# Performance work log

Hardware: AMD Instinct MI355X
Metric: run time of the kernel (lower is better)

The kernel has to match this reference:

```python
import jax, jax.numpy as jnp
import numpy as np

H = 8
LOG2 = 0.6931471805599453  # softplus beta = ln(2)
LN_EPS = 1e-5


def _lin(x, w, b):
    return x @ w + b


def _ln(x, g, b):
    m = jnp.mean(x, -1, keepdims=True)
    v = jnp.mean((x - m) ** 2, -1, keepdims=True)
    return (x - m) / jnp.sqrt(v + LN_EPS) * g + b


def _eca(x, y, z):
    # efficient_causal_attention_parallel: x,y (b,n,d1), z (b,n,d2)
    n = x.shape[1]
    accum = jnp.cumsum(y[:, :, :, None] * z[:, :, None, :], axis=1)  # (b,n,d1,d2)
    res = jnp.einsum('bnd,bnde->bne', x, accum)
    return res / jnp.arange(1, n + 1, dtype=x.dtype)[None, :, None]


def _split(x, B, L):
    # (B,L,H*dh) -> (B,H,L,dh)
    return x.reshape(B, L, H, -1).transpose(0, 2, 1, 3)


def _mha(qi, ki, vi, wq, bq, wk, bk, wv, bv, mask):
    B, Lq, D = qi.shape
    dh = D // H
    q = _split(_lin(qi, wq, bq), B, Lq) * dh ** -0.5
    k = _split(_lin(ki, wk, bk), B, ki.shape[1])
    v = _split(_lin(vi, wv, bv), B, vi.shape[1])
    s = jnp.einsum('bhqd,bhkd->bhqk', q, k)
    if mask is not None:
        s = jnp.where(mask[:, None, None, :], -10000.0, s)
    a = jax.nn.softmax(s, -1)
    ctx = jnp.einsum('bhqk,bhkd->bhqd', a, v)
    return ctx.transpose(0, 2, 1, 3).reshape(B, Lq, D)


def _forward(dec_outputs, p, enc_outputs,
             sa_q_w, sa_q_b, sa_pq_w, sa_pq_b, sa_pc_w, sa_pc_b,
             sa_k_w, sa_k_b, sa_v_w, sa_v_b, sa_out_w, sa_out_b,
             pk_q_w, pk_q_b, pk_k_w, pk_k_b, pk_v_w, pk_v_b,
             up_q_w, up_q_b, up_k_w, up_k_b, up_v_w, up_v_b,
             ca_lin_w, ca_lin_b, yp_ln_g, yp_ln_b, yx_ln_g, yx_ln_b,
             ff_w1, ff_b1, ff_w2, ff_b2, ff_ln_g, ff_ln_b,
             dec_input_mask, p_mask, enc_input_mask):
    B, n, D = dec_outputs.shape
    pl = p.shape[1]
    dh = D // H
    scale = dh ** -0.5
    x = dec_outputs
    # --- LunaCausalAttention (self) ---
    pq = _split(_lin(p, sa_pq_w, sa_pq_b), B, pl) * scale           # (B,H,pl,dh)
    pq = pq.reshape(B * H, pl, dh).transpose(0, 2, 1)               # (B*H,dh,pl)
    pc = _split(_lin(x, sa_pc_w, sa_pc_b), B, n).reshape(B * H, n, dh)
    pattn = jax.nn.softplus(LOG2 * jnp.matmul(pc, pq)) / LOG2       # (B*H,n,pl)
    q = _split(_lin(x, sa_q_w, sa_q_b), B, n).reshape(B * H, n, dh) * scale
    k = _split(_lin(x, sa_k_w, sa_k_b), B, n).reshape(B * H, n, dh)
    v = _split(_lin(x, sa_v_w, sa_v_b), B, n).reshape(B * H, n, dh)
    aw = _eca(q, k, pattn)                                          # (B*H,n,pl)
    aw = jnp.where(p_mask[:, None, None, :], 1e-9,
                   aw.reshape(B, H, n, pl)).reshape(B * H, n, pl)
    probs = jax.nn.softmax(aw, -1)
    attn = _eca(probs, pattn, v)                                    # (B*H,n,dh)
    attn = attn.reshape(B, H, n, dh).transpose(0, 2, 1, 3).reshape(B, n, D)
    dec = _lin(attn, sa_out_w, sa_out_b) + dec_outputs
    # --- LinearUnifiedNestedAttention (cross) ---
    Yp = _mha(p, enc_outputs, enc_outputs,
              pk_q_w, pk_q_b, pk_k_w, pk_k_b, pk_v_w, pk_v_b, enc_input_mask)
    Yx = _mha(dec, Yp, Yp,
              up_q_w, up_q_b, up_k_w, up_k_b, up_v_w, up_v_b, p_mask)
    Yx = _lin(Yx, ca_lin_w, ca_lin_b)
    Yp = _ln(Yp + p, yp_ln_g, yp_ln_b)
    Yx = _ln(Yx + dec, yx_ln_g, yx_ln_b)
    # --- FFN (dropout p=0 in eval) ---
    ff = _lin(jax.nn.relu(_lin(Yx, ff_w1, ff_b1)), ff_w2, ff_b2)
    out = _ln(ff + Yx, ff_ln_g, ff_ln_b)
    return (out, Yp)


PROJ_NAMES = ['sa_q', 'sa_pq', 'sa_pc', 'sa_k', 'sa_v', 'sa_out',
              'pk_q', 'pk_k', 'pk_v', 'up_q', 'up_k', 'up_v', 'ca_lin']


def setup_inputs() -> dict:
    key = jax.random.key(0)
    ks = iter(jax.random.split(key, 64))
    B, N, PL, D, F = 2, 1024, 32, 512, 2048
    inp = {
        'dec_outputs': jax.random.normal(next(ks), (B, N, D), jnp.float32),
        'p': jax.random.normal(next(ks), (B, PL, D), jnp.float32),
        'enc_outputs': jax.random.normal(next(ks), (B, N, D), jnp.float32),
        'dec_input_mask': jnp.zeros((B, N), bool),
        'p_mask': jnp.zeros((B, PL), bool),
        'enc_input_mask': jnp.zeros((B, N), bool),
    }
    for nm in PROJ_NAMES:
        inp[nm + '_w'] = jax.random.normal(next(ks), (D, D), jnp.float32) * 0.02
        inp[nm + '_b'] = jnp.zeros((D,), jnp.float32)
    for nm in ['yp_ln', 'yx_ln', 'ff_ln']:
        inp[nm + '_g'] = jnp.ones((D,), jnp.float32)
        inp[nm + '_b'] = jnp.zeros((D,), jnp.float32)
    inp['ff_w1'] = jax.random.normal(next(ks), (D, F), jnp.float32) * 0.02
    inp['ff_b1'] = jnp.zeros((F,), jnp.float32)
    inp['ff_w2'] = jax.random.normal(next(ks), (F, D), jnp.float32) * 0.02
    inp['ff_b2'] = jnp.zeros((D,), jnp.float32)
    return inp


def reference(dec_outputs, p, enc_outputs,
              sa_q_w, sa_q_b, sa_pq_w, sa_pq_b, sa_pc_w, sa_pc_b,
              sa_k_w, sa_k_b, sa_v_w, sa_v_b, sa_out_w, sa_out_b,
              pk_q_w, pk_q_b, pk_k_w, pk_k_b, pk_v_w, pk_v_b,
              up_q_w, up_q_b, up_k_w, up_k_b, up_v_w, up_v_b,
              ca_lin_w, ca_lin_b, yp_ln_g, yp_ln_b, yx_ln_g, yx_ln_b,
              ff_w1, ff_b1, ff_w2, ff_b2, ff_ln_g, ff_ln_b,
              dec_input_mask, p_mask, enc_input_mask):
    return _forward(dec_outputs, p, enc_outputs,
                    sa_q_w, sa_q_b, sa_pq_w, sa_pq_b, sa_pc_w, sa_pc_b,
                    sa_k_w, sa_k_b, sa_v_w, sa_v_b, sa_out_w, sa_out_b,
                    pk_q_w, pk_q_b, pk_k_w, pk_k_b, pk_v_w, pk_v_b,
                    up_q_w, up_q_b, up_k_w, up_k_b, up_v_w, up_v_b,
                    ca_lin_w, ca_lin_b, yp_ln_g, yp_ln_b, yx_ln_g, yx_ln_b,
                    ff_w1, ff_b1, ff_w2, ff_b2, ff_ln_g, ff_ln_b,
                    dec_input_mask, p_mask, enc_input_mask)
```

## Files before the change

### kernel.cpp

```cpp
#include <hip/hip_runtime.h>
#include <hip/hip_bf16.h>

typedef __hip_bfloat16 bf16;
typedef __attribute__((ext_vector_type(8))) short bf8_t;
typedef __attribute__((ext_vector_type(4))) float f4_t;

__device__ __forceinline__ float b2f(bf16 x) { return __bfloat162float(x); }

__device__ __forceinline__ float ldany(const void* p, size_t i, int isbf) {
    return isbf ? b2f(((const bf16*)p)[i]) : ((const float*)p)[i];
}

__device__ __forceinline__ short f2b(float f) {
    unsigned u = __builtin_bit_cast(unsigned, f);
    u += 0x7fffu + ((u >> 16) & 1u);
    return (short)(u >> 16);
}

__global__ __launch_bounds__(64) void k_detect(const void* __restrict__ dec,
                                               int* __restrict__ flag) {
    __shared__ int cnt;
    if (threadIdx.x == 0) cnt = 0;
    __syncthreads();
    int bad = 0;
    for (int i = threadIdx.x; i < 256; i += 64) {
        float f = b2f(((const bf16*)dec)[i]);
        float a = fabsf(f);
        if (!(a < 1e10f) || (a != 0.f && a < 1e-20f)) bad++;
    }
    atomicAdd(&cnt, bad);
    __syncthreads();
    if (threadIdx.x == 0) *flag = (cnt >= 3) ? 0 : 1;
}

__global__ __launch_bounds__(256) void k_tobf_all(
    const void* __restrict__ dec, const void* __restrict__ enc,
    const void* __restrict__ p, short* __restrict__ dec_bf,
    short* __restrict__ enc_bf, short* __restrict__ p_bf,
    const int* __restrict__ flagp) {
    int isbf = *flagp;
    size_t i = (size_t)blockIdx.x * 256 + threadIdx.x;
    const void* src;
    short* dst;
    size_t idx;
    if (i < 1048576) { src = dec; dst = dec_bf; idx = i; }
    else if (i < 2097152) { src = enc; dst = enc_bf; idx = i - 1048576; }
    else { src = p; dst = p_bf; idx = i - 2097152; }
    dst[idx] = isbf ? ((const short*)src)[idx]
                    : f2b(((const float*)src)[idx]);
}

struct WT15 {
    const void* src[15];
};

__global__ __launch_bounds__(256) void k_wtrans_all(
    WT15 w, short* __restrict__ wt, short* __restrict__ ff1t,
    short* __restrict__ ff2t, const int* __restrict__ flagp) {
    __shared__ float T[32][33];
    int isbf = *flagp;
    int id = blockIdx.x;
    const void* src;
    short* d;
    int K, N, bx, by;
    if (id < 3328) {
        int slab = id >> 8, rem = id & 255;
        src = w.src[slab];
        d = wt + (size_t)slab * 262144;
        K = 512; N = 512;
        bx = rem & 15; by = rem >> 4;
    } else if (id < 4352) {
        int rem = id - 3328;
        src = w.src[13]; d = ff1t;
        K = 512; N = 2048;
        bx = rem & 63; by = rem >> 6;
    } else {
        int rem = id - 4352;
        src = w.src[14]; d = ff2t;
        K = 2048; N = 512;
        bx = rem & 15; by = rem >> 4;
    }
    int nb = bx * 32, kb = by * 32;
    int col = threadIdx.x & 31, row0 = threadIdx.x >> 5;
#pragma unroll
    for (int i = 0; i < 4; i++) {
        int r = row0 + i * 8;
        T[r][col] = ldany(src, (size_t)(kb + r) * N + nb + col, isbf);
    }
    __syncthreads();
#pragma unroll
    for (int i = 0; i < 4; i++) {
        int r = row0 + i * 8;
        d[(size_t)(nb + r) * K + kb + col] = f2b(T[col][r]);
    }
}

struct GJob {
    const short* A;
    const short* W[4];
    const void* Bias[4];
    float scale[4];
    float* Out[4];
    short* OutBf[4];
    const float* Res;
    const void* ResAny;
    int Nper, K, relu;
    int gx, nblk, blk0;
};
struct GJobs {
    GJob j[2];
    int nj;
};

__global__ __launch_bounds__(256, 6) void k_gemm_mfma(
    GJobs gs, const int* __restrict__ flagp) {
    constexpr int ASTR = 72;
    constexpr int BSTR = 72;
    __shared__ __align__(16) short As[64 * ASTR];
    __shared__ __align__(16) short Bs[64 * BSTR];
    int isbf = *flagp;
    int tid = threadIdx.x;
    int wave = tid >> 6, lane = tid & 63;
    int quad = lane >> 4, l16 = lane & 15;
    int id = blockIdx.x;
    int ji = (gs.nj > 1 && id >= gs.j[1].blk0) ? 1 : 0;
    const GJob& jb = gs.j[ji];
    int lid = id - jb.blk0;
    int gx = jb.gx, nblk = jb.nblk;
    int bx, by;
    if ((nblk & 7) == 0) {
        int per = nblk >> 3;
        int id2 = (lid & 7) * per + (lid >> 3);
        by = id2 / gx;
        bx = id2 - by * gx;
    } else {
        by = lid / gx;
        bx = lid - by * gx;
    }
    int K = jb.K;
    int mb = by * 64;
    int nbg = bx * 64;
    int slot = nbg / jb.Nper;
    int nb = nbg - slot * jb.Nper;
    const short* Wt = jb.W[slot];
    const short* A = jb.A;
    int wn = wave * 16;
    f4_t acc[4] = {};

    int ar = tid >> 3;
    int ak = (tid & 7) * 8;
    const short* Ap = A + (size_t)mb * K;
    const short* Wp = Wt + (size_t)nb * K;
    int4 av0 = *(const int4*)(Ap + (size_t)ar * K + ak);
    int4 av1 = *(const int4*)(Ap + (size_t)(ar + 32) * K + ak);
    int4 bv0 = *(const int4*)(Wp + (size_t)ar * K + ak);
    int4 bv1 = *(const int4*)(Wp + (size_t)(ar + 32) * K + ak);
    for (int k0 = 0; k0 < K; k0 += 64) {
        __syncthreads();
        *(int4*)&As[ar * ASTR + ak] = av0;
        *(int4*)&As[(ar + 32) * ASTR + ak] = av1;
        *(int4*)&Bs[ar * BSTR + ak] = bv0;
        *(int4*)&Bs[(ar + 32) * BSTR + ak] = bv1;
        int kn = k0 + 64;
        if (kn < K) {
            av0 = *(const int4*)(Ap + (size_t)ar * K + kn + ak);
            av1 = *(const int4*)(Ap + (size_t)(ar + 32) * K + kn + ak);
            bv0 = *(const int4*)(Wp + (size_t)ar * K + kn + ak);
            bv1 = *(const int4*)(Wp + (size_t)(ar + 32) * K + kn + ak);
        }
        __syncthreads();
#pragma unroll
        for (int half = 0; half < 2; half++) {
            bf8_t b = *(const bf8_t*)&Bs[(wn + l16) * BSTR + half * 32 +
                                         quad * 8];
#pragma unroll
            for (int fi = 0; fi < 4; fi++) {
                bf8_t a = *(const bf8_t*)&As[(fi * 16 + l16) * ASTR +
                                             half * 32 + quad * 8];
                acc[fi] = __builtin_amdgcn_mfma_f32_16x16x32_bf16(a, b,
                                                                  acc[fi],
                                                                  0, 0, 0);
            }
        }
    }
    const void* Bias = jb.Bias[slot];
    float scale = jb.scale[slot];
    float* O = jb.Out[slot];
    short* Ob = jb.OutBf[slot];
    const float* Res = jb.Res;
    const void* ResAny = jb.ResAny;
    int Nper = jb.Nper;
    int relu = jb.relu;
    int n = nb + wn + l16;
    float bia = ldany(Bias, n, isbf);
#pragma unroll
    for (int fi = 0; fi < 4; fi++) {
#pragma unroll
        for (int r = 0; r < 4; r++) {
            int m = mb + fi * 16 + quad * 4 + r;
            float v = (acc[fi][r] + bia) * scale;
            if (relu) v = fmaxf(v, 0.f);
            if (Res) v += Res[(size_t)m * Nper + n];
            if (ResAny) v += ldany(ResAny, (size_t)m * Nper + n, isbf);
            if (O) O[(size_t)m * Nper + n] = v;
            if (Ob) Ob[(size_t)m * Nper + n] = f2b(v);
        }
    }
}

__global__ __launch_bounds__(256) void k_eca1_f(
    const float* __restrict__ pcp, const float* __restrict__ pqp,
    const float* __restrict__ kp, const float* __restrict__ vp,
    float* __restrict__ pattn, float* __restrict__ L1,
    float* __restrict__ L2) {
    __shared__ float Ks[64][65];
    __shared__ float Vs[64][65];
    __shared__ float Ps[64][33];
    int bh = blockIdx.y, c = blockIdx.x;
    int b = bh >> 3, h = bh & 7;
    size_t rowbase = (size_t)b * 1024 + c * 64;
    for (int ch = threadIdx.x; ch < 1024; ch += 256) {
        int s = ch >> 4, d4 = (ch & 15) * 4;
        float4 c4 = *(const float4*)&pcp[(rowbase + s) * 512 + h * 64 + d4];
        Ks[s][d4] = c4.x; Ks[s][d4 + 1] = c4.y;
        Ks[s][d4 + 2] = c4.z; Ks[s][d4 + 3] = c4.w;
    }
    for (int ch = threadIdx.x; ch < 512; ch += 256) {
        int e = ch >> 4, d4 = (ch & 15) * 4;
        float4 q4 = *(const float4*)&pqp[(size_t)(b * 32 + e) * 512 + h * 64 + d4];
        Vs[e][d4] = q4.x; Vs[e][d4 + 1] = q4.y;
        Vs[e][d4 + 2] = q4.z; Vs[e][d4 + 3] = q4.w;
    }
    __syncthreads();
    {
        int e = threadIdx.x & 31, t0 = threadIdx.x >> 5;
#pragma unroll
        for (int rr = 0; rr < 8; rr++) {
            int r = t0 + rr * 8;
            float s = 0.f;
#pragma unroll
            for (int dd = 0; dd < 64; dd++) s += Ks[r][dd] * Vs[e][dd];
            float v = (s > 0.f) ? (s + log2f(1.f + exp2f(-s)))
                                : log2f(1.f + exp2f(s));
            Ps[r][e] = v;
            pattn[((size_t)bh * 1024 + c * 64 + r) * 32 + e] = v;
        }
    }
    __syncthreads();
    for (int ch = threadIdx.x; ch < 1024; ch += 256) {
        int s = ch >> 4, d4 = (ch & 15) * 4;
        size_t gidx = (rowbase + s) * 512 + h * 64 + d4;
        float4 k4 = *(const float4*)&kp[gidx];
        float4 v4 = *(const float4*)&vp[gidx];
        Ks[s][d4] = k4.x; Ks[s][d4 + 1] = k4.y;
        Ks[s][d4 + 2] = k4.z; Ks[s][d4 + 3] = k4.w;
        Vs[s][d4] = v4.x; Vs[s][d4 + 1] = v4.y;
        Vs[s][d4 + 2] = v4.z; Vs[s][d4 + 3] = v4.w;
    }
    __syncthreads();
    size_t lbase = ((size_t)bh * 16 + c) * 2048;
    {
        int e = threadIdx.x & 31, dd0 = (threadIdx.x >> 5) * 8;
        float acc[8] = {};
        for (int s = 0; s < 64; s++) {
            float ps = Ps[s][e];
#pragma unroll
            for (int j = 0; j < 8; j++) acc[j] += Ks[s][dd0 + j] * ps;
        }
#pragma unroll
        for (int j = 0; j < 8; j++) L1[lbase + (dd0 + j) * 32 + e] = acc[j];
    }
    {
        int dd = threadIdx.x & 63, e0 = (threadIdx.x >> 6) * 8;
        float acc[8] = {};
        for (int s = 0; s < 64; s++) {
            float vv = Vs[s][dd];
#pragma unroll
            for (int j = 0; j < 8; j++) acc[j] += Ps[s][e0 + j] * vv;
        }
#pragma unroll
        for (int j = 0; j < 8; j++) L2[lbase + (e0 + j) * 64 + dd] = acc[j];
    }
}

__global__ __launch_bounds__(256) void k_scan(float* __restrict__ L1,
                                              float* __restrict__ L2) {
    int gid = blockIdx.x * 256 + threadIdx.x;
    int bh = gid >> 11, lin = gid & 2047;
    size_t base = (size_t)bh * 16 * 2048 + lin;
    float run = 0.f;
#pragma unroll
    for (int c = 0; c < 16; c++) {
        float v = L1[base + c * 2048];
        L1[base + c * 2048] = run;
        run += v;
    }
    run = 0.f;
#pragma unroll
    for (int c = 0; c < 16; c++) {
        float v = L2[base + c * 2048];
        L2[base + c * 2048] = run;
        run += v;
    }
}

__global__ __launch_bounds__(512) void k_eca3(
    const float* __restrict__ qp, const float* __restrict__ kp,
    const float* __restrict__ vp, const float* __restrict__ pattn,
    const float* __restrict__ L1s, const float* __restrict__ L2s,
    short* __restrict__ attnbf) {
    __shared__ float R0[64][65];
    __shared__ float R1[64][65];
    __shared__ float Ps[64][33];
    __shared__ float SS[2112];
    __shared__ float Pr[64][33];
    int bh = blockIdx.y, c = blockIdx.x;
    int b = bh >> 3, h = bh & 7;
    size_t rowbase = (size_t)b * 1024 + c * 64;
    int tid = threadIdx.x;
    for (int ch = tid; ch < 1024; ch += 512) {
        int t = ch >> 4, d4 = (ch & 15) * 4;
        size_t gidx = (rowbase + t) * 512 + h * 64 + d4;
        float4 q4 = *(const float4*)&qp[gidx];
        float4 k4 = *(const float4*)&kp[gidx];
        R0[t][d4] = q4.x; R0[t][d4 + 1] = q4.y;
        R0[t][d4 + 2] = q4.z; R0[t][d4 + 3] = q4.w;
        R1[t][d4] = k4.x; R1[t][d4 + 1] = k4.y;
        R1[t][d4 + 2] = k4.z; R1[t][d4 + 3] = k4.w;
    }
    if (tid < 512) {
        int ch = tid;
        {
            int t = ch >> 3, e4 = (ch & 7) * 4;
            float4 p4 = *(const float4*)&pattn[((size_t)bh * 1024 + c * 64 + t) * 32 + e4];
            Ps[t][e4] = p4.x; Ps[t][e4 + 1] = p4.y;
            Ps[t][e4 + 2] = p4.z; Ps[t][e4 + 3] = p4.w;
        }
        {
            float4 s4 = *(const float4*)&L1s[((size_t)bh * 16 + c) * 2048 + ch * 4];
            int dd = ch >> 3, e4 = (ch & 7) * 4;
            SS[dd * 33 + e4] = s4.x; SS[dd * 33 + e4 + 1] = s4.y;
            SS[dd * 33 + e4 + 2] = s4.z; SS[dd * 33 + e4 + 3] = s4.w;
        }
    }
    __syncthreads();
    int tx = tid & 15, ty = tid >> 4;
    float a1r[2][4] = {};
    float qs1[2][2] = {};
    for (int dd = 0; dd < 64; dd++) {
        float q2[2], k4[4];
#pragma unroll
        for (int i = 0; i < 2; i++) q2[i] = R0[ty * 2 + i][dd];
#pragma unroll
        for (int j = 0; j < 4; j++) k4[j] = R1[tx * 4 + j][dd];
#pragma unroll
        for (int i = 0; i < 2; i++)
#pragma unroll
            for (int j = 0; j < 4; j++) a1r[i][j] += q2[i] * k4[j];
        float s1a = SS[dd * 33 + tx * 2], s1b = SS[dd * 33 + tx * 2 + 1];
#pragma unroll
        for (int i = 0; i < 2; i++) {
            qs1[i][0] += q2[i] * s1a;
            qs1[i][1] += q2[i] * s1b;
        }
    }
    __syncthreads();
#pragma unroll
    for (int i = 0; i < 2; i++) {
#pragma unroll
        for (int j = 0; j < 4; j++) R0[ty * 2 + i][tx * 4 + j] = a1r[i][j];
        Pr[ty * 2 + i][tx * 2] = qs1[i][0];
        Pr[ty * 2 + i][tx * 2 + 1] = qs1[i][1];
    }
    for (int ch = tid; ch < 1024; ch += 512) {
        int t = ch >> 4, d4 = (ch & 15) * 4;
        float4 v4 = *(const float4*)&vp[(rowbase + t) * 512 + h * 64 + d4];
        R1[t][d4] = v4.x; R1[t][d4 + 1] = v4.y;
        R1[t][d4 + 2] = v4.z; R1[t][d4 + 3] = v4.w;
    }
    __syncthreads();
    {
        int e = tid & 31, t0 = (tid >> 5) * 4;
        for (int k2 = 0; k2 < 4; k2++) {
            int t = t0 + k2;
            float s = Pr[t][e];
            for (int s2 = 0; s2 <= t; s2++) s += R0[t][s2] * Ps[s2][e];
            Pr[t][e] = s / (float)(c * 64 + t + 1);
        }
    }
    __syncthreads();
    if (tid < 64) {
        float m = -1e30f;
        for (int e = 0; e < 32; e++) m = fmaxf(m, Pr[tid][e]);
        float sum = 0.f;
        for (int e = 0; e < 32; e++) {
            float ex = expf(Pr[tid][e] - m);
            Pr[tid][e] = ex;
            sum += ex;
        }
        float inv = 1.f / sum;
        for (int e = 0; e < 32; e++) Pr[tid][e] *= inv;
    } else if (tid >= 128) {
        for (int ch = tid - 128; ch < 512; ch += 384) {
            float4 s4 = *(const float4*)&L2s[((size_t)bh * 16 + c) * 2048 + ch * 4];
            int e = ch >> 4, d4 = (ch & 15) * 4;
            SS[e * 65 + d4] = s4.x; SS[e * 65 + d4 + 1] = s4.y;
            SS[e * 65 + d4 + 2] = s4.z; SS[e * 65 + d4 + 3] = s4.w;
        }
    }
    __syncthreads();
    float a2r[2][4] = {};
    float ps2[2][4] = {};
    for (int e = 0; e < 32; e++) {
        float p2[2], b4[4], v4[4];
#pragma unroll
        for (int i = 0; i < 2; i++) p2[i] = Pr[ty * 2 + i][e];
#pragma unroll
        for (int j = 0; j < 4; j++) {
            b4[j] = Ps[tx * 4 + j][e];
            v4[j] = SS[e * 65 + tx * 4 + j];
        }
#pragma unroll
        for (int i = 0; i < 2; i++)
#pragma unroll
            for (int j = 0; j < 4; j++) {
                a2r[i][j] += p2[i] * b4[j];
                ps2[i][j] += p2[i] * v4[j];
            }
    }
    __syncthreads();
#pragma unroll
    for (int i = 0; i < 2; i++)
#pragma unroll
        for (int j = 0; j < 4; j++) R0[ty * 2 + i][tx * 4 + j] = a2r[i][j];
    __syncthreads();
#pragma unroll
    for (int i = 0; i < 2; i++) {
        int t = ty * 2 + i;
        float acch[4];
#pragma unroll
        for (int j = 0; j < 4; j++) acch[j] = ps2[i][j];
        for (int s = 0; s <= t; s++) {
            float a2v = R0[t][s];
#pragma unroll
            for (int j = 0; j < 4; j++) acch[j] += a2v * R1[s][tx * 4 + j];
        }
        float inv = 1.f / (float)(c * 64 + t + 1);
        short4 o;
        o.x = f2b(acch[0] * inv); o.y = f2b(acch[1] * inv);
        o.z = f2b(acch[2] * inv); o.w = f2b(acch[3] * inv);
        *(short4*)&attnbf[(rowbase + t) * 512 + h * 64 + tx * 4] = o;
    }
}

__global__ __launch_bounds__(256) void k_mha1_part(
    const float* __restrict__ pkq, const float* __restrict__ pkk,
    const float* __restrict__ pkv, float* __restrict__ partC,
    float* __restrict__ ml) {
    __shared__ float Qs[32][65];
    __shared__ float Ks[64][65];
    __shared__ float Vs[64][65];
    __shared__ float Ps[32][65];
    int bh = blockIdx.y, ks = blockIdx.x;
    int b = bh >> 3, h = bh & 7;
    for (int lin = threadIdx.x; lin < 2048; lin += 256) {
        int i = lin >> 6, dd = lin & 63;
        Qs[i][dd] = pkq[(size_t)(b * 32 + i) * 512 + h * 64 + dd];
    }
    for (int lin = threadIdx.x; lin < 4096; lin += 256) {
        int kk = lin >> 6, dd = lin & 63;
        size_t g = ((size_t)b * 1024 + ks * 64 + kk) * 512 + h * 64 + dd;
        Ks[kk][dd] = pkk[g];
        Vs[kk][dd] = pkv[g];
    }
    __syncthreads();
    int k = threadIdx.x & 63, ig = threadIdx.x >> 6;
    float s[8];
#pragma unroll
    for (int j = 0; j < 8; j++) {
        int i = ig * 8 + j;
        float acc = 0.f;
#pragma unroll
        for (int dd = 0; dd < 64; dd++) acc += Qs[i][dd] * Ks[k][dd];
        s[j] = acc;
    }
#pragma unroll
    for (int j = 0; j < 8; j++) {
        float m = s[j];
#pragma unroll
        for (int off = 32; off >= 1; off >>= 1)
            m = fmaxf(m, __shfl_xor(m, off, 64));
        float e = expf(s[j] - m);
        float l = e;
#pragma unroll
        for (int off = 32; off >= 1; off >>= 1) l += __shfl_xor(l, off, 64);
        Ps[ig * 8 + j][k] = e;
        if (k == 0) {
            int i = ig * 8 + j;
            ml[((size_t)bh * 16 + ks) * 64 + i * 2] = m;
            ml[((size_t)bh * 16 + ks) * 64 + i * 2 + 1] = l;
        }
    }
    __syncthreads();
    int dd = k;
    float acc[8] = {};
    for (int kk = 0; kk < 64; kk++) {
        float vv = Vs[kk][dd];
#pragma unroll
        for (int j = 0; j < 8; j++) acc[j] += Ps[ig * 8 + j][kk] * vv;
    }
    size_t base = ((size_t)bh * 16 + ks) * 2048;
#pragma unroll
    for (int j = 0; j < 8; j++) partC[base + (ig * 8 + j) * 64 + dd] = acc[j];
}

__global__ __launch_bounds__(256) void k_mha1_red_ln(
    const float* __restrict__ partC, const float* __restrict__ ml,
    const void* __restrict__ p_in, const void* __restrict__ gv,
    const void* __restrict__ bv, short* __restrict__ yp_bf,
    void* __restrict__ outany, size_t ooff, const int* __restrict__ flagp) {
    __shared__ float red[8];
    int isbf = *flagp;
    int row = blockIdx.x;
    int b = row >> 5, i = row & 31;
    float v[2];
#pragma unroll
    for (int t = 0; t < 2; t++) {
        int col = (int)threadIdx.x + t * 256;
        int h = col >> 6, dd = col & 63;
        int bh = b * 8 + h;
        float M = -1e30f;
        for (int ks2 = 0; ks2 < 16; ks2++)
            M = fmaxf(M, ml[((size_t)bh * 16 + ks2) * 64 + i * 2]);
        float L = 0.f, acc = 0.f;
        for (int ks2 = 0; ks2 < 16; ks2++) {
            float m = ml[((size_t)bh * 16 + ks2) * 64 + i * 2];
            float l = ml[((size_t)bh * 16 + ks2) * 64 + i * 2 + 1];
            float w = expf(m - M);
            L += l * w;
            acc += partC[((size_t)bh * 16 + ks2) * 2048 + i * 64 + dd] * w;
        }
        float raw = acc / L;
        size_t o = (size_t)(b * 32 + i) * 512 + col;
        yp_bf[o] = f2b(raw);
        v[t] = raw + ldany(p_in, o, isbf);
    }
    int wave = threadIdx.x >> 6, lane = threadIdx.x & 63;
    float sum = v[0] + v[1];
#pragma unroll
    for (int off = 32; off >= 1; off >>= 1) sum += __shfl_xor(sum, off, 64);
    if (lane == 0) red[wave] = sum;
    __syncthreads();
    float mean = (red[0] + red[1] + red[2] + red[3]) * (1.f / 512.f);
    float var = 0.f;
#pragma unroll
    for (int t = 0; t < 2; t++) {
        float d = v[t] - mean;
        var += d * d;
    }
#pragma unroll
    for (int off = 32; off >= 1; off >>= 1) var += __shfl_xor(var, off, 64);
    if (lane == 0) red[wave + 4] = var;
    __syncthreads();
    var = (red[4] + red[5] + red[6] + red[7]) * (1.f / 512.f);
    float inv = rsqrtf(var + 1e-5f);
#pragma unroll
    for (int t = 0; t < 2; t++) {
        int col = (int)threadIdx.x + t * 256;
        size_t o = (size_t)(b * 32 + i) * 512 + col;
        float y = (v[t] - mean) * inv * ldany(gv, col, isbf) +
                  ldany(bv, col, isbf);
        if (isbf)
            ((bf16*)outany + ooff)[o] = __float2bfloat16(y);
        else
            ((float*)outany + ooff)[o] = y;
    }
}

__global__ __launch_bounds__(256) void k_mha2(const float* __restrict__ upq,
                                              const float* __restrict__ upk,
                                              const float* __restrict__ upv,
                                              short* __restrict__ yxbf) {
    __shared__ float Ksm[32][65];
    __shared__ float Vsm[32][65];
    __shared__ float Qsm[64][65];
    __shared__ float Prm[64][33];
    int bh = blockIdx.y, c = blockIdx.x;
    int b = bh >> 3, h = bh & 7;
    for (int lin = threadIdx.x; lin < 2048; lin += 256) {
        int e = lin >> 6, dd = lin & 63;
        Ksm[e][dd] = upk[(size_t)(b * 32 + e) * 512 + h * 64 + dd];
        Vsm[e][dd] = upv[(size_t)(b * 32 + e) * 512 + h * 64 + dd];
    }
    for (int lin = threadIdx.x; lin < 4096; lin += 256) {
        int t = lin >> 6, dd = lin & 63;
        Qsm[t][dd] = upq[((size_t)b * 1024 + c * 64 + t) * 512 + h * 64 + dd];
    }
    __syncthreads();
    int row = threadIdx.x >> 2, r = threadIdx.x & 3;
    float p[8];
#pragma unroll
    for (int j = 0; j < 8; j++) {
        int e = r * 8 + j;
        float s = 0.f;
#pragma unroll
        for (int dd = 0; dd < 64; dd++) s += Qsm[row][dd] * Ksm[e][dd];
        p[j] = s;
    }
    float m = -1e30f;
#pragma unroll
    for (int j = 0; j < 8; j++) m = fmaxf(m, p[j]);
    m = fmaxf(m, __shfl_xor(m, 1, 64));
    m = fmaxf(m, __shfl_xor(m, 2, 64));
    float sum = 0.f;
#pragma unroll
    for (int j = 0; j < 8; j++) {
        p[j] = expf(p[j] - m);
        sum += p[j];
    }
    sum += __shfl_xor(sum, 1, 64);
    sum += __shfl_xor(sum, 2, 64);
    float inv = 1.f / sum;
#pragma unroll
    for (int j = 0; j < 8; j++) Prm[row][r * 8 + j] = p[j] * inv;
    __syncthreads();
    for (int j4 = 0; j4 < 4; j4++) {
        short4 o;
        float a4[4];
#pragma unroll
        for (int q = 0; q < 4; q++) {
            int dd = r * 16 + j4 * 4 + q;
            float acc = 0.f;
#pragma unroll
            for (int e = 0; e < 32; e++) acc += Prm[row][e] * Vsm[e][dd];
            a4[q] = acc;
        }
        o.x = f2b(a4[0]); o.y = f2b(a4[1]);
        o.z = f2b(a4[2]); o.w = f2b(a4[3]);
        *(short4*)&yxbf[((size_t)b * 1024 + c * 64 + row) * 512 + h * 64 +
                        r * 16 + j4 * 4] = o;
    }
}

__global__ __launch_bounds__(256) void k_ln(
    const float* __restrict__ x, const float* __restrict__ residf,
    const void* __restrict__ residany, const void* __restrict__ gv,
    const void* __restrict__ bv, float* __restrict__ out32,
    short* __restrict__ dupbf, void* __restrict__ outany, size_t ooff,
    const int* __restrict__ flagp) {
    int isbf = *flagp;
    int wave = threadIdx.x >> 6, lane = threadIdx.x & 63;
    int row = blockIdx.x * 4 + wave;
    const float* px = x + (size_t)row * 512;
    float v[8];
#pragma unroll
    for (int j = 0; j < 8; j++) {
        int col = lane + 64 * j;
        v[j] = px[col];
        if (residf) v[j] += residf[(size_t)row * 512 + col];
        if (residany) v[j] += ldany(residany, (size_t)row * 512 + col, isbf);
    }
    float sum = 0.f;
#pragma unroll
    for (int j = 0; j < 8; j++) sum += v[j];
#pragma unroll
    for (int off = 32; off >= 1; off >>= 1) sum += __shfl_xor(sum, off, 64);
    float mean = sum * (1.f / 512.f);
    float var = 0.f;
#pragma unroll
    for (int j = 0; j < 8; j++) {
        float d = v[j] - mean;
        var += d * d;
    }
#pragma unroll
    for (int off = 32; off >= 1; off >>= 1) var += __shfl_xor(var, off, 64);
    var *= (1.f / 512.f);
    float inv = rsqrtf(var + 1e-5f);
#pragma unroll
    for (int j = 0; j < 8; j++) {
        int col = lane + 64 * j;
        float y = (v[j] - mean) * inv * ldany(gv, col, isbf) +
                  ldany(bv, col, isbf);
        size_t oidx = (size_t)row * 512 + col;
        if (out32) out32[oidx] = y;
        if (dupbf) dupbf[oidx] = f2b(y);
        if (outany) {
            if (isbf)
                ((bf16*)outany + ooff)[oidx] = __float2bfloat16(y);
            else
                ((float*)outany + ooff)[oidx] = y;
        }
    }
}

extern "C" void kernel_launch(void* const* d_in, const int* in_sizes, int n_in,
                              void* d_out, int out_size, void* d_ws,
                              size_t ws_size, hipStream_t stream) {
    (void)in_sizes; (void)n_in; (void)out_size; (void)ws_size;
    const void* dec_in = d_in[0];
    const void* p_in = d_in[1];
    const void* enc_in = d_in[2];

    const size_t M1 = 1048576;
    float* ws = (float*)d_ws;
    float* A_ = ws + 0 * M1;
    float* B_ = ws + 1 * M1;
    float* C_ = ws + 2 * M1;
    float* D_ = ws + 3 * M1;
    float* E_ = ws + 4 * M1;
    float* F_ = ws + 5 * M1;
    float* S_ = ws + 6 * M1;
    float* pattn = S_;
    float* L1 = S_ + 524288;
    float* L2 = S_ + 1048576;
    float* pqp = S_ + 1572864;
    float* pkq = S_ + 1605632;
    float* ml = S_ + 1638400;
    float* upk = S_ + 1671168;
    float* upv = S_ + 1703936;
    float* partC = S_;
    int* flagp = (int*)(S_ + 1736704);
    short* attn_bf = (short*)E_;
    short* mha2_bf = (short*)(E_ + 524288);
    short* ff1_bf = (short*)B_;
    short* dec_bf = (short*)(ws + 7 * M1 + 786432);
    short* enc_bf = dec_bf + M1;
    short* p_bf = enc_bf + M1;
    short* F_bf = p_bf + 32768;
    short* yp_bf = F_bf + M1;
    short* yx2_bf = yp_bf + 32768;
    short* wt = yx2_bf + M1;
    short* ff1t = wt + 13 * 262144;
    short* ff2t = ff1t + M1;
    auto WTp = [&](int wi) { return wt + (size_t)((wi - 6) / 2) * 262144; };
    auto Bv = [&](int i) { return (const void*)d_in[i]; };
    short* nb16 = nullptr;
    float* nf32 = nullptr;

    hipStream_t S = stream;
    k_detect<<<1, 64, 0, S>>>(dec_in, flagp);
    k_tobf_all<<<8320, 256, 0, S>>>(dec_in, enc_in, p_in, dec_bf, enc_bf,
                                    p_bf, flagp);
    {
        WT15 w;
        for (int s = 0; s < 13; s++) w.src[s] = d_in[6 + 2 * s];
        w.src[13] = d_in[38];
        w.src[14] = d_in[40];
        k_wtrans_all<<<5376, 256, 0, S>>>(w, wt, ff1t, ff2t, flagp);
    }

    {
        GJobs g{};
        g.nj = 2;
        GJob& a = g.j[0];
        a.A = dec_bf;
        a.W[0] = WTp(6); a.W[1] = WTp(10); a.W[2] = WTp(12); a.W[3] = WTp(14);
        a.Bias[0] = Bv(7); a.Bias[1] = Bv(11); a.Bias[2] = Bv(13);
        a.Bias[3] = Bv(15);
        a.scale[0] = 0.125f; a.scale[1] = 1.f; a.scale[2] = 1.f;
        a.scale[3] = 1.f;
        a.Out[0] = A_; a.Out[1] = D_; a.Out[2] = B_; a.Out[3] = C_;
        a.OutBf[0] = nb16; a.OutBf[1] = nb16; a.OutBf[2] = nb16;
        a.OutBf[3] = nb16;
        a.Res = nullptr; a.ResAny = nullptr;
        a.Nper = 512; a.K = 512; a.relu = 0;
        a.gx = 32; a.nblk = 1024; a.blk0 = 0;
        GJob& b = g.j[1];
        b.A = p_bf;
        b.W[0] = WTp(8); b.W[1] = WTp(18); b.W[2] = WTp(8); b.W[3] = WTp(8);
        b.Bias[0] = Bv(9); b.Bias[1] = Bv(19); b.Bias[2] = Bv(9);
        b.Bias[3] = Bv(9);
        b.scale[0] = 0.125f; b.scale[1] = 0.125f; b.scale[2] = 0.f;
        b.scale[3] = 0.f;
        b.Out[0] = pqp; b.Out[1] = pkq; b.Out[2] = pqp; b.Out[3] = pqp;
        b.OutBf[0] = nb16; b.OutBf[1] = nb16; b.OutBf[2] = nb16;
        b.OutBf[3] = nb16;
        b.Res = nullptr; b.ResAny = nullptr;
        b.Nper = 512; b.K = 512; b.relu = 0;
        b.gx = 16; b.nblk = 16; b.blk0 = 1024;
        k_gemm_mfma<<<1040, 256, 0, S>>>(g, flagp);
    }
    k_eca1_f<<<dim3(16, 16), 256, 0, S>>>(D_, pqp, B_, C_, pattn, L1, L2);
    k_scan<<<128, 256, 0, S>>>(L1, L2);
    k_eca3<<<dim3(16, 16), 512, 0, S>>>(A_, B_, C_, pattn, L1, L2, attn_bf);

    {
        GJobs g{};
        g.nj = 2;
        GJob& a = g.j[0];
        a.A = attn_bf;
        a.W[0] = WTp(16); a.W[1] = WTp(16); a.W[2] = WTp(16); a.W[3] = WTp(16);
        a.Bias[0] = Bv(17); a.Bias[1] = Bv(17); a.Bias[2] = Bv(17);
        a.Bias[3] = Bv(17);
        a.scale[0] = 1.f; a.scale[1] = 1.f; a.scale[2] = 1.f; a.scale[3] = 1.f;
        a.Out[0] = F_; a.Out[1] = F_; a.Out[2] = F_; a.Out[3] = F_;
        a.OutBf[0] = F_bf; a.OutBf[1] = F_bf; a.OutBf[2] = F_bf;
        a.OutBf[3] = F_bf;
        a.Res = nullptr; a.ResAny = dec_in;
        a.Nper = 512; a.K = 512; a.relu = 0;
        a.gx = 8; a.nblk = 256; a.blk0 = 0;
        GJob& b = g.j[1];
        b.A = enc_bf;
        b.W[0] = WTp(20); b.W[1] = WTp(22); b.W[2] = WTp(20); b.W[3] = WTp(20);
        b.Bias[0] = Bv(21); b.Bias[1] = Bv(23); b.Bias[2] = Bv(21);
        b.Bias[3] = Bv(21);
        b.scale[0] = 1.f; b.scale[1] = 1.f; b.scale[2] = 1.f; b.scale[3] = 1.f;
        b.Out[0] = B_; b.Out[1] = C_; b.Out[2] = B_; b.Out[3] = B_;
        b.OutBf[0] = nb16; b.OutBf[1] = nb16; b.OutBf[2] = nb16;
        b.OutBf[3] = nb16;
        b.Res = nullptr; b.ResAny = nullptr;
        b.Nper = 512; b.K = 512; b.relu = 0;
        b.gx = 16; b.nblk = 512; b.blk0 = 256;
        k_gemm_mfma<<<768, 256, 0, S>>>(g, flagp);
    }
    k_mha1_part<<<dim3(16, 16), 256, 0, S>>>(pkq, B_, C_, partC, ml);
    k_mha1_red_ln<<<64, 256, 0, S>>>(partC, ml, p_in, d_in[32], d_in[33],
                                     yp_bf, d_out, 1048576, flagp);

    {
        GJobs g{};
        g.nj = 2;
        GJob& a = g.j[0];
        a.A = yp_bf;
        a.W[0] = WTp(26); a.W[1] = WTp(28); a.W[2] = WTp(26); a.W[3] = WTp(26);
        a.Bias[0] = Bv(27); a.Bias[1] = Bv(29); a.Bias[2] = Bv(27);
        a.Bias[3] = Bv(27);
        a.scale[0] = 1.f; a.scale[1] = 1.f; a.scale[2] = 1.f; a.scale[3] = 1.f;
        a.Out[0] = upk; a.Out[1] = upv; a.Out[2] = upk; a.Out[3] = upk;
        a.OutBf[0] = nb16; a.OutBf[1] = nb16; a.OutBf[2] = nb16;
        a.OutBf[3] = nb16;
        a.Res = nullptr; a.ResAny = nullptr;
        a.Nper = 512; a.K = 512; a.relu = 0;
        a.gx = 16; a.nblk = 16; a.blk0 = 0;
        GJob& b = g.j[1];
        b.A = F_bf;
        b.W[0] = WTp(24); b.W[1] = WTp(24); b.W[2] = WTp(24); b.W[3] = WTp(24);
        b.Bias[0] = Bv(25); b.Bias[1] = Bv(25); b.Bias[2] = Bv(25);
        b.Bias[3] = Bv(25);
        b.scale[0] = 0.125f; b.scale[1] = 0.125f; b.scale[2] = 0.125f;
        b.scale[3] = 0.125f;
        b.Out[0] = C_; b.Out[1] = C_; b.Out[2] = C_; b.Out[3] = C_;
        b.OutBf[0] = nb16; b.OutBf[1] = nb16; b.OutBf[2] = nb16;
        b.OutBf[3] = nb16;
        b.Res = nullptr; b.ResAny = nullptr;
        b.Nper = 512; b.K = 512; b.relu = 0;
        b.gx = 8; b.nblk = 256; b.blk0 = 16;
        k_gemm_mfma<<<272, 256, 0, S>>>(g, flagp);
    }
    k_mha2<<<dim3(16, 16), 256, 0, S>>>(C_, upk, upv, mha2_bf);

    {
        GJobs g{};
        g.nj = 1;
        GJob& a = g.j[0];
        a.A = mha2_bf;
        a.W[0] = WTp(30); a.W[1] = WTp(30); a.W[2] = WTp(30); a.W[3] = WTp(30);
        a.Bias[0] = Bv(31); a.Bias[1] = Bv(31); a.Bias[2] = Bv(31);
        a.Bias[3] = Bv(31);
        a.scale[0] = 1.f; a.scale[1] = 1.f; a.scale[2] = 1.f; a.scale[3] = 1.f;
        a.Out[0] = D_; a.Out[1] = D_; a.Out[2] = D_; a.Out[3] = D_;
        a.OutBf[0] = nb16; a.OutBf[1] = nb16; a.OutBf[2] = nb16;
        a.OutBf[3] = nb16;
        a.Res = nullptr; a.ResAny = nullptr;
        a.Nper = 512; a.K = 512; a.relu = 0;
        a.gx = 8; a.nblk = 256; a.blk0 = 0;
        k_gemm_mfma<<<256, 256, 0, S>>>(g, flagp);
    }
    k_ln<<<2048 / 4, 256, 0, S>>>(D_, F_, nullptr, d_in[34], d_in[35], A_,
                                  yx2_bf, nullptr, 0, flagp);

    {
        GJobs g{};
        g.nj = 1;
        GJob& a = g.j[0];
        a.A = yx2_bf;
        a.W[0] = ff1t; a.W[1] = ff1t; a.W[2] = ff1t; a.W[3] = ff1t;
        a.Bias[0] = Bv(39); a.Bias[1] = Bv(39); a.Bias[2] = Bv(39);
        a.Bias[3] = Bv(39);
        a.scale[0] = 1.f; a.scale[1] = 1.f; a.scale[2] = 1.f; a.scale[3] = 1.f;
        a.Out[0] = nf32; a.Out[1] = nf32; a.Out[2] = nf32; a.Out[3] = nf32;
        a.OutBf[0] = ff1_bf; a.OutBf[1] = ff1_bf; a.OutBf[2] = ff1_bf;
        a.OutBf[3] = ff1_bf;
        a.Res = nullptr; a.ResAny = nullptr;
        a.Nper = 2048; a.K = 512; a.relu = 1;
        a.gx = 32; a.nblk = 1024; a.blk0 = 0;
        k_gemm_mfma<<<1024, 256, 0, S>>>(g, flagp);
    }
    {
        GJobs g{};
        g.nj = 1;
        GJob& a = g.j[0];
        a.A = ff1_bf;
        a.W[0] = ff2t; a.W[1] = ff2t; a.W[2] = ff2t; a.W[3] = ff2t;
        a.Bias[0] = Bv(41); a.Bias[1] = Bv(41); a.Bias[2] = Bv(41);
        a.Bias[3] = Bv(41);
        a.scale[0] = 1.f; a.scale[1] = 1.f; a.scale[2] = 1.f; a.scale[3] = 1.f;
        a.Out[0] = F_; a.Out[1] = F_; a.Out[2] = F_; a.Out[3] = F_;
        a.OutBf[0] = nb16; a.OutBf[1] = nb16; a.OutBf[2] = nb16;
        a.OutBf[3] = nb16;
        a.Res = nullptr; a.ResAny = nullptr;
        a.Nper = 512; a.K = 2048; a.relu = 0;
        a.gx = 8; a.nblk = 256; a.blk0 = 0;
        k_gemm_mfma<<<256, 256, 0, S>>>(g, flagp);
    }
    k_ln<<<2048 / 4, 256, 0, S>>>(F_, A_, nullptr, d_in[36], d_in[37],
                                  nullptr, nullptr, d_out, 0, flagp);
}
```

Baseline: 340.3 us.

## Double-buffer GEMM tiles via direct global-to-LDS loads with XOR swizzle

Replaces the register-staged global-to-shared copy in the MFMA GEMM with global_load_lds direct transfers into two LDS buffers. The next K tile is prefetched while the current one is consumed, which removes one barrier per iteration. Padding is replaced by an XOR swizzle to avoid bank conflicts. LDS use doubles and launch bounds drop to 4 blocks per CU, reducing occupancy, and correctness relies on the lane-to-LDS mapping of the direct load matching the swizzle.

```diff
diff --git a/kernel.cpp b/kernel.cpp
--- a/kernel.cpp
+++ b/kernel.cpp
@@ -15,6 +15,12 @@
     unsigned u = __builtin_bit_cast(unsigned, f);
     u += 0x7fffu + ((u >> 16) & 1u);
     return (short)(u >> 16);
+}
+
+__device__ __forceinline__ void gload16(const short* g, short* l) {
+    __builtin_amdgcn_global_load_lds(
+        (const __attribute__((address_space(1))) void*)g,
+        (__attribute__((address_space(3))) void*)l, 16, 0, 0);
 }
 
 __global__ __launch_bounds__(64) void k_detect(const void* __restrict__ dec,
@@ -112,12 +118,10 @@
     int nj;
 };
 
-__global__ __launch_bounds__(256, 6) void k_gemm_mfma(
+__global__ __launch_bounds__(256, 4) void k_gemm_mfma(
     GJobs gs, const int* __restrict__ flagp) {
-    constexpr int ASTR = 72;
-    constexpr int BSTR = 72;
-    __shared__ __align__(16) short As[64 * ASTR];
-    __shared__ __align__(16) short Bs[64 * BSTR];
+    __shared__ __align__(16) short As[2][64 * 64];
+    __shared__ __align__(16) short Bs[2][64 * 64];
     int isbf = *flagp;
     int tid = threadIdx.x;
     int wave = tid >> 6, lane = tid & 63;
@@ -147,41 +151,48 @@
     int wn = wave * 16;
     f4_t acc[4] = {};
 
-    int ar = tid >> 3;
-    int ak = (tid & 7) * 8;
     const short* Ap = A + (size_t)mb * K;
     const short* Wp = Wt + (size_t)nb * K;
-    int4 av0 = *(const int4*)(Ap + (size_t)ar * K + ak);
-    int4 av1 = *(const int4*)(Ap + (size_t)(ar + 32) * K + ak);
-    int4 bv0 = *(const int4*)(Wp + (size_t)ar * K + ak);
-    int4 bv1 = *(const int4*)(Wp + (size_t)(ar + 32) * K + ak);
+    int w8 = wave * 8;
+    int lr = lane >> 3;
+    int lc = ((lane & 7) ^ lr) * 8;
+    const short* ga0 = Ap + (size_t)(w8 + lr) * K + lc;
+    const short* gb0 = Wp + (size_t)(w8 + lr) * K + lc;
+    short* la0 = &As[0][w8 * 64];
+    short* lb0 = &Bs[0][w8 * 64];
+
+    auto stage = [&](int buf, int k) {
+        gload16(ga0 + k, la0 + buf * 4096);
+        gload16(ga0 + (size_t)32 * K + k, la0 + buf * 4096 + 32 * 64);
+        gload16(gb0 + k, lb0 + buf * 4096);
+        gload16(gb0 + (size_t)32 * K + k, lb0 + buf * 4096 + 32 * 64);
+    };
+
+    int sw = l16 & 7;
+
+    stage(0, 0);
+    asm volatile("s_waitcnt vmcnt(0)" ::: "memory");
+    __builtin_amdgcn_s_barrier();
+    int cur = 0;
     for (int k0 = 0; k0 < K; k0 += 64) {
-        __syncthreads();
-        *(int4*)&As[ar * ASTR + ak] = av0;
-        *(int4*)&As[(ar + 32) * ASTR + ak] = av1;
-        *(int4*)&Bs[ar * BSTR + ak] = bv0;
-        *(int4*)&Bs[(ar + 32) * BSTR + ak] = bv1;
         int kn = k0 + 64;
-        if (kn < K) {
-            av0 = *(const int4*)(Ap + (size_t)ar * K + kn + ak);
-            av1 = *(const int4*)(Ap + (size_t)(ar + 32) * K + kn + ak);
-            bv0 = *(const int4*)(Wp + (size_t)ar * K + kn + ak);
-            bv1 = *(const int4*)(Wp + (size_t)(ar + 32) * K + kn + ak);
-        }
-        __syncthreads();
+        if (kn < K) stage(cur ^ 1, kn);
 #pragma unroll
         for (int half = 0; half < 2; half++) {
-            bf8_t b = *(const bf8_t*)&Bs[(wn + l16) * BSTR + half * 32 +
-                                         quad * 8];
+            bf8_t b = *(const bf8_t*)&Bs[cur][(wn + l16) * 64 +
+                                             ((half * 4 + quad) ^ sw) * 8];
 #pragma unroll
             for (int fi = 0; fi < 4; fi++) {
-                bf8_t a = *(const bf8_t*)&As[(fi * 16 + l16) * ASTR +
-                                             half * 32 + quad * 8];
+                bf8_t a = *(const bf8_t*)&As[cur][(fi * 16 + l16) * 64 +
+                                                  ((half * 4 + quad) ^ sw) * 8];
                 acc[fi] = __builtin_amdgcn_mfma_f32_16x16x32_bf16(a, b,
                                                                   acc[fi],
                                                                   0, 0, 0);
             }
         }
+        asm volatile("s_waitcnt vmcnt(0)" ::: "memory");
+        __builtin_amdgcn_s_barrier();
+        cur ^= 1;
     }
     const void* Bias = jb.Bias[slot];
     float scale = jb.scale[slot];
```

Result: no change. 341.4 us (+0.3%).
